# Kernel tuning notes

Hardware: AMD Instinct MI355X
Metric: run time of the kernel (lower is better)

The kernel has to match this reference:

```python
import jax, jax.numpy as jnp
import numpy as np

B = 131072
RES_DIM = 100
N_CHAMBERS = 6
CF_ITERS = 5
CF_K = 0.02

COUPLING = np.array([
    [0.0, -0.3, 0.6, 0.4, -0.2, 0.3],
    [-0.3, 0.0, -0.5, -0.7, 0.6, 0.4],
    [0.6, -0.5, 0.0, 0.3, -0.3, 0.2],
    [0.4, -0.7, 0.3, 0.0, -0.4, 0.5],
    [-0.2, 0.6, -0.3, -0.4, 0.0, 0.3],
    [0.3, 0.4, 0.2, 0.5, 0.3, 0.0],
], dtype=np.float32)
DECAY = np.array([0.9, 0.93, 0.85, 0.97, 0.88, 0.94], dtype=np.float32)


def setup_inputs() -> dict:
    key = jax.random.key(0)
    ks = jax.random.split(key, 9)
    def lin(k, fan_in, fan_out):
        kw, kb = jax.random.split(k)
        bound = 1.0 / np.sqrt(fan_in)
        W = jax.random.uniform(kw, (N_CHAMBERS, fan_in, fan_out), jnp.float32, -bound, bound)
        b = jax.random.uniform(kb, (N_CHAMBERS, fan_out), jnp.float32, -bound, bound)
        return W, b
    W1, b1 = lin(ks[0], RES_DIM, 128)
    W2, b2 = lin(ks[1], 128, 64)
    W3, b3 = lin(ks[2], 64, 32)
    W4, b4 = lin(ks[3], 32, 1)
    W4 = W4[:, :, 0]  # (6, 32)
    b4 = b4[:, 0]     # (6,)
    res = jax.random.normal(ks[4], (B, RES_DIM), jnp.float32)
    return {
        "res": res,
        "W1": W1, "b1": b1, "W2": W2, "b2": b2,
        "W3": W3, "b3": b3, "W4": W4, "b4": b4,
        "coupling": jnp.asarray(COUPLING),
        "decay": jnp.asarray(DECAY),
    }


def reference(res, W1, b1, W2, b2, W3, b3, W4, b4, coupling, decay):
    # 6 per-chamber MLP towers, batched over the chamber axis c.
    h = jax.nn.silu(jnp.einsum('bd,cdh->cbh', res, W1) + b1[:, None, :])   # (6,B,128)
    h = jax.nn.silu(jnp.einsum('cbh,cho->cbo', h, W2) + b2[:, None, :])    # (6,B,64)
    h = jax.nn.silu(jnp.einsum('cbh,cho->cbo', h, W3) + b3[:, None, :])    # (6,B,32)
    raw = (jnp.einsum('cbh,ch->cb', h, W4) + b4[:, None]).T                # (B,6)
    # 5-step coupled sigmoid recurrence on the tiny (B,6) state.
    act = jax.nn.sigmoid(raw)
    for _ in range(CF_ITERS):
        delta = ((act * decay) @ coupling) * CF_K
        act = jax.nn.sigmoid(raw + delta)
    return act, raw
```

## Files before the change

### kernel.cpp

```cpp
#include <hip/hip_runtime.h>
#include <hip/hip_bf16.h>
#include <stdint.h>

#define B_TOTAL 131072

typedef __attribute__((ext_vector_type(8))) short short8;
typedef __attribute__((ext_vector_type(16))) float float16v;

#define CH_U16 24576
#define oF2 14336
#define oF3 22528
#define BF16_TOT (6 * CH_U16)
#define F32_BASE (BF16_TOT / 2)
#define sB1 0
#define sB2 768
#define sB3 1152
#define sW4 1344
#define sB4 1536
#define sCP 1542
#define sDC 1578
#define NSMALL 1584
#define CONV_TOT (BF16_TOT + NSMALL)

#define GLB_AS __attribute__((address_space(1)))
#define LDS_AS __attribute__((address_space(3)))

__device__ __forceinline__ float bf16_as_f32(uint16_t u) {
    union { uint32_t i; float f; } v; v.i = ((uint32_t)u) << 16; return v.f;
}
__device__ __forceinline__ uint16_t f2bf(float f) {
    uint32_t u = __float_as_uint(f);
    return (uint16_t)((u + 0x7FFFu + ((u >> 16) & 1u)) >> 16);
}
__device__ __forceinline__ float sigmoidf_fast(float x) {
    return __builtin_amdgcn_rcpf(1.0f + __expf(-x));
}
__device__ __forceinline__ float siluf(float x) { return x * sigmoidf_fast(x); }

__device__ __forceinline__ float readsrc(const void* p, int off, bool bf) {
    return bf ? bf16_as_f32(((const uint16_t*)p)[off]) : ((const float*)p)[off];
}

__device__ __forceinline__ uint32_t cvtpk_bf16(float lo, float hi) {
    uint32_t r;
    asm("v_cvt_pk_bf16_f32 %0, %1, %2" : "=v"(r) : "v"(lo), "v"(hi));
    return r;
}
__device__ __forceinline__ void plane32swap(uint32_t& a, uint32_t& b) {
    asm("v_permlane32_swap_b32 %0, %1" : "+v"(a), "+v"(b));
}

__global__ void convert_kernel(const void* W1, const void* b1, const void* W2, const void* b2,
                               const void* W3, const void* b3, const void* W4, const void* b4,
                               const void* cp, const void* dc, uint16_t* __restrict__ wsb) {
    const bool bf = (((const uint32_t*)cp)[0] != 0u);
    int idx = blockIdx.x * 256 + threadIdx.x;
    if (idx >= CONV_TOT) return;
    if (idx < BF16_TOT) {
        int c = idx / CH_U16;
        int r = idx - c * CH_U16;
        float v;
        if (r < oF2) {
            int f = r >> 9, rem = r & 511, l = rem >> 3, e = rem & 7;
            int ct = f / 7, kb = f - ct * 7;
            int n = ct * 32 + (l & 31), k = kb * 16 + (l >> 5) * 8 + e;
            v = (k < 100) ? readsrc(W1, c * 12800 + k * 128 + n, bf) : 0.0f;
        } else if (r < oF3) {
            int j = r - oF2;
            int f = j >> 9, rem = j & 511, l = rem >> 3, e = rem & 7;
            int ct2 = f >> 3, kb = f & 7;
            int n = ct2 * 32 + (l & 31), k = kb * 16 + (l >> 5) * 8 + e;
            v = readsrc(W2, c * 8192 + k * 64 + n, bf);
        } else {
            int j = r - oF3;
            int kb = j >> 9, rem = j & 511, l = rem >> 3, e = rem & 7;
            int n = (l & 31), k = kb * 16 + (l >> 5) * 8 + e;
            v = readsrc(W3, c * 2048 + k * 32 + n, bf);
        }
        wsb[idx] = f2bf(v);
    } else {
        int fi = idx - BF16_TOT;
        float v;
        if      (fi < sB2)  v = readsrc(b1, fi, bf);
        else if (fi < sB3)  v = readsrc(b2, fi - sB2, bf);
        else if (fi < sW4)  v = readsrc(b3, fi - sB3, bf);
        else if (fi < sB4)  v = readsrc(W4, fi - sW4, bf);
        else if (fi < sCP)  v = readsrc(b4, fi - sB4, bf);
        else if (fi < sDC)  v = readsrc(cp, fi - sCP, bf);
        else                v = readsrc(dc, fi - sDC, bf);
        ((float*)wsb)[F32_BASE + fi] = v;
    }
}

union Frag { uint4 u4; uint2 u2[2]; uint32_t u[4]; short8 s8; uint16_t h[8]; };

#define Z16 {0.f,0.f,0.f,0.f,0.f,0.f,0.f,0.f,0.f,0.f,0.f,0.f,0.f,0.f,0.f,0.f}

__global__ __launch_bounds__(512, 4)
void chambers_mfma(const void* __restrict__ resv, const uint16_t* __restrict__ wsb,
                   const uint32_t* __restrict__ cpw, float* __restrict__ outF) {
    const float* wsf = (const float*)wsb;
    const bool bfin = (cpw[0] != 0u);
    const int tid = threadIdx.x;
    const int w = tid >> 6, l = tid & 63;
    const int l5 = l & 31, q2 = l >> 5;
    const int row = blockIdx.x * 256 + w * 32 + l5;

    __shared__ __align__(16) uint16_t sW[CH_U16];
    __shared__ __align__(16) float sB[NSMALL];

    for (int i = tid; i < NSMALL; i += 512) sB[i] = wsf[F32_BASE + i];

    Frag R[7];
    if (bfin) {
        const uint16_t* bp = (const uint16_t*)resv + (size_t)row * 100;
#pragma unroll
        for (int kb = 0; kb < 6; ++kb) {
            const int k0 = kb * 16 + q2 * 8;
            R[kb].u2[0] = *(const uint2*)(bp + k0);
            R[kb].u2[1] = *(const uint2*)(bp + k0 + 4);
        }
        R[6].u4 = make_uint4(0, 0, 0, 0);
        if (q2 == 0) R[6].u2[0] = *(const uint2*)(bp + 96);
    } else {
        const float* fp = (const float*)resv + (size_t)row * 100;
#pragma unroll
        for (int kb = 0; kb < 6; ++kb) {
            const int k0 = kb * 16 + q2 * 8;
            float4 x0 = *(const float4*)(fp + k0);
            float4 x1 = *(const float4*)(fp + k0 + 4);
            R[kb].u[0] = cvtpk_bf16(x0.x, x0.y);
            R[kb].u[1] = cvtpk_bf16(x0.z, x0.w);
            R[kb].u[2] = cvtpk_bf16(x1.x, x1.y);
            R[kb].u[3] = cvtpk_bf16(x1.z, x1.w);
        }
        R[6].u4 = make_uint4(0, 0, 0, 0);
        if (q2 == 0) {
            float4 x0 = *(const float4*)(fp + 96);
            R[6].u[0] = cvtpk_bf16(x0.x, x0.y);
            R[6].u[1] = cvtpk_bf16(x0.z, x0.w);
        }
    }

    float raw0 = 0.f, raw1 = 0.f, raw2 = 0.f, raw3 = 0.f, raw4 = 0.f, raw5 = 0.f;
    uint32_t pk1[16][2];
    uint32_t pk2[8][2];

#pragma unroll 1
    for (int c = 0; c < 6; ++c) {
        if (c) __syncthreads();
        {
            const uint16_t* gsrc = wsb + c * CH_U16;
#pragma unroll
            for (int r = 0; r < 6; ++r) {
                const int chunk = r * 8 + w;
                __builtin_amdgcn_global_load_lds(
                    (const GLB_AS uint32_t*)(gsrc + chunk * 512 + l * 8),
                    (LDS_AS uint32_t*)(sW + chunk * 512),
                    16, 0, 0);
            }
        }
        __syncthreads();

#pragma unroll
        for (int ct = 0; ct < 4; ++ct) {
            float16v acc = Z16;
#pragma unroll
            for (int kb = 0; kb < 7; ++kb) {
                Frag Af; Af.u4 = *(const uint4*)(sW + ((ct * 7 + kb) * 64 + l) * 8);
                acc = __builtin_amdgcn_mfma_f32_32x32x16_bf16(Af.s8, R[kb].s8, acc, 0, 0, 0);
            }
#pragma unroll
            for (int ar = 0; ar < 4; ++ar) {
                const float4 bv = *(const float4*)(sB + sB1 + c * 128 + ct * 32 + ar * 8 + q2 * 4);
                pk1[ct * 4 + ar][0] = cvtpk_bf16(siluf(acc[4 * ar + 0] + bv.x),
                                                 siluf(acc[4 * ar + 1] + bv.y));
                pk1[ct * 4 + ar][1] = cvtpk_bf16(siluf(acc[4 * ar + 2] + bv.z),
                                                 siluf(acc[4 * ar + 3] + bv.w));
            }
        }
#pragma unroll
        for (int ct2 = 0; ct2 < 2; ++ct2) {
            float16v acc = Z16;
#pragma unroll
            for (int kb = 0; kb < 8; ++kb) {
                uint32_t x0 = pk1[2 * kb][0], y0 = pk1[2 * kb + 1][0];
                uint32_t x1 = pk1[2 * kb][1], y1 = pk1[2 * kb + 1][1];
                plane32swap(x0, y0);
                plane32swap(x1, y1);
                Frag Hf; Hf.u[0] = x0; Hf.u[1] = x1; Hf.u[2] = y0; Hf.u[3] = y1;
                Frag Af; Af.u4 = *(const uint4*)(sW + oF2 + ((ct2 * 8 + kb) * 64 + l) * 8);
                acc = __builtin_amdgcn_mfma_f32_32x32x16_bf16(Af.s8, Hf.s8, acc, 0, 0, 0);
            }
#pragma unroll
            for (int ar = 0; ar < 4; ++ar) {
                const float4 bv = *(const float4*)(sB + sB2 + c * 64 + ct2 * 32 + ar * 8 + q2 * 4);
                pk2[ct2 * 4 + ar][0] = cvtpk_bf16(siluf(acc[4 * ar + 0] + bv.x),
                                                  siluf(acc[4 * ar + 1] + bv.y));
                pk2[ct2 * 4 + ar][1] = cvtpk_bf16(siluf(acc[4 * ar + 2] + bv.z),
                                                  siluf(acc[4 * ar + 3] + bv.w));
            }
        }
        {
            float16v acc = Z16;
#pragma unroll
            for (int kb = 0; kb < 4; ++kb) {
                uint32_t x0 = pk2[2 * kb][0], y0 = pk2[2 * kb + 1][0];
                uint32_t x1 = pk2[2 * kb][1], y1 = pk2[2 * kb + 1][1];
                plane32swap(x0, y0);
                plane32swap(x1, y1);
                Frag Hf; Hf.u[0] = x0; Hf.u[1] = x1; Hf.u[2] = y0; Hf.u[3] = y1;
                Frag Af; Af.u4 = *(const uint4*)(sW + oF3 + (kb * 64 + l) * 8);
                acc = __builtin_amdgcn_mfma_f32_32x32x16_bf16(Af.s8, Hf.s8, acc, 0, 0, 0);
            }
            float part = 0.f;
#pragma unroll
            for (int ar = 0; ar < 4; ++ar) {
                const float4 bv = *(const float4*)(sB + sB3 + c * 32 + ar * 8 + q2 * 4);
                const float4 wv = *(const float4*)(sB + sW4 + c * 32 + ar * 8 + q2 * 4);
                part = fmaf(siluf(acc[4 * ar + 0] + bv.x), wv.x, part);
                part = fmaf(siluf(acc[4 * ar + 1] + bv.y), wv.y, part);
                part = fmaf(siluf(acc[4 * ar + 2] + bv.z), wv.z, part);
                part = fmaf(siluf(acc[4 * ar + 3] + bv.w), wv.w, part);
            }
            part += __shfl_xor(part, 32);
            const float rv = part + sB[sB4 + c];
            raw0 = (c == 0) ? rv : raw0;
            raw1 = (c == 1) ? rv : raw1;
            raw2 = (c == 2) ? rv : raw2;
            raw3 = (c == 3) ? rv : raw3;
            raw4 = (c == 4) ? rv : raw4;
            raw5 = (c == 5) ? rv : raw5;
        }
    }

    const float rv6[6] = {raw0, raw1, raw2, raw3, raw4, raw5};
    float av[6];
#pragma unroll
    for (int c = 0; c < 6; ++c) av[c] = sigmoidf_fast(rv6[c]);
    const float K = 0.02f;
#pragma unroll 1
    for (int it = 0; it < 5; ++it) {
        float tt[6];
#pragma unroll
        for (int i = 0; i < 6; ++i) tt[i] = av[i] * sB[sDC + i] * K;
#pragma unroll
        for (int j = 0; j < 6; ++j) {
            float dl = 0.0f;
#pragma unroll
            for (int i = 0; i < 6; ++i) dl = fmaf(tt[i], sB[sCP + i * 6 + j], dl);
            av[j] = sigmoidf_fast(rv6[j] + dl);
        }
    }
    if (q2 == 0) {
        float2* oa = (float2*)(outF + (size_t)row * 6);
        oa[0] = make_float2(av[0], av[1]);
        oa[1] = make_float2(av[2], av[3]);
        oa[2] = make_float2(av[4], av[5]);
        float2* orw = (float2*)(outF + (size_t)B_TOTAL * 6 + (size_t)row * 6);
        orw[0] = make_float2(rv6[0], rv6[1]);
        orw[1] = make_float2(rv6[2], rv6[3]);
        orw[2] = make_float2(rv6[4], rv6[5]);
    }
}

extern "C" void kernel_launch(void* const* d_in, const int* in_sizes, int n_in,
                              void* d_out, int out_size, void* d_ws, size_t ws_size,
                              hipStream_t stream) {
    uint16_t* wsb = (uint16_t*)d_ws;
    convert_kernel<<<(CONV_TOT + 255) / 256, 256, 0, stream>>>(
        d_in[1], d_in[2], d_in[3], d_in[4], d_in[5], d_in[6], d_in[7], d_in[8],
        d_in[9], d_in[10], wsb);
    chambers_mfma<<<B_TOTAL / 256, 512, 0, stream>>>(
        d_in[0], wsb, (const uint32_t*)d_in[9], (float*)d_out);
}
```

Before: 163.5 us.

## Load layer-2 weights directly from global into registers and seed accumulators with biases

Layer-2 weight fragments now go straight from global memory (L2-cached) into registers instead of being staged through LDS. LDS staging is cut to layer-1 and layer-3 weights, which shrinks shared memory from 48KB to 32KB per block. MFMA accumulators are initialised with the bias values, so the bias adds after each GEMM go away. The aim is to lower LDS traffic and footprint, which could allow more resident blocks. The cost is more VGPR pressure from 8 live uint4 fragments and global-load latency inside the chamber loop.

```diff
diff --git a/kernel.cpp b/kernel.cpp
--- a/kernel.cpp
+++ b/kernel.cpp
@@ -21,6 +21,8 @@
 #define sDC 1578
 #define NSMALL 1584
 #define CONV_TOT (BF16_TOT + NSMALL)
+
+#define sWF3 14336
 
 #define GLB_AS __attribute__((address_space(1)))
 #define LDS_AS __attribute__((address_space(3)))
@@ -94,8 +96,6 @@
 
 union Frag { uint4 u4; uint2 u2[2]; uint32_t u[4]; short8 s8; uint16_t h[8]; };
 
-#define Z16 {0.f,0.f,0.f,0.f,0.f,0.f,0.f,0.f,0.f,0.f,0.f,0.f,0.f,0.f,0.f,0.f}
-
 __global__ __launch_bounds__(512, 4)
 void chambers_mfma(const void* __restrict__ resv, const uint16_t* __restrict__ wsb,
                    const uint32_t* __restrict__ cpw, float* __restrict__ outF) {
@@ -106,7 +106,7 @@
     const int l5 = l & 31, q2 = l >> 5;
     const int row = blockIdx.x * 256 + w * 32 + l5;
 
-    __shared__ __align__(16) uint16_t sW[CH_U16];
+    __shared__ __align__(16) uint16_t sW[16384];
     __shared__ __align__(16) float sB[NSMALL];
 
     for (int i = tid; i < NSMALL; i += 512) sB[i] = wsf[F32_BASE + i];
@@ -152,19 +152,32 @@
         {
             const uint16_t* gsrc = wsb + c * CH_U16;
 #pragma unroll
-            for (int r = 0; r < 6; ++r) {
-                const int chunk = r * 8 + w;
+            for (int r = 0; r < 4; ++r) {
+                const int i = r * 8 + w;
+                const int gi = (i < 28) ? i : (i + 16);
                 __builtin_amdgcn_global_load_lds(
-                    (const GLB_AS uint32_t*)(gsrc + chunk * 512 + l * 8),
-                    (LDS_AS uint32_t*)(sW + chunk * 512),
+                    (const GLB_AS uint32_t*)(gsrc + gi * 512 + l * 8),
+                    (LDS_AS uint32_t*)(sW + i * 512),
                     16, 0, 0);
             }
         }
         __syncthreads();
 
+        const uint16_t* gF2 = wsb + c * CH_U16 + oF2;
+        Frag F2a[8];
+#pragma unroll
+        for (int kb = 0; kb < 8; ++kb)
+            F2a[kb].u4 = *(const uint4*)(gF2 + (kb * 64 + l) * 8);
+
 #pragma unroll
         for (int ct = 0; ct < 4; ++ct) {
-            float16v acc = Z16;
+            float16v acc;
+#pragma unroll
+            for (int ar = 0; ar < 4; ++ar) {
+                const float4 bv = *(const float4*)(sB + sB1 + c * 128 + ct * 32 + ar * 8 + q2 * 4);
+                acc[4 * ar + 0] = bv.x; acc[4 * ar + 1] = bv.y;
+                acc[4 * ar + 2] = bv.z; acc[4 * ar + 3] = bv.w;
+            }
 #pragma unroll
             for (int kb = 0; kb < 7; ++kb) {
                 Frag Af; Af.u4 = *(const uint4*)(sW + ((ct * 7 + kb) * 64 + l) * 8);
@@ -172,37 +185,56 @@
             }
 #pragma unroll
             for (int ar = 0; ar < 4; ++ar) {
-                const float4 bv = *(const float4*)(sB + sB1 + c * 128 + ct * 32 + ar * 8 + q2 * 4);
-                pk1[ct * 4 + ar][0] = cvtpk_bf16(siluf(acc[4 * ar + 0] + bv.x),
-                                                 siluf(acc[4 * ar + 1] + bv.y));
-                pk1[ct * 4 + ar][1] = cvtpk_bf16(siluf(acc[4 * ar + 2] + bv.z),
-                                                 siluf(acc[4 * ar + 3] + bv.w));
-            }
-        }
-#pragma unroll
-        for (int ct2 = 0; ct2 < 2; ++ct2) {
-            float16v acc = Z16;
-#pragma unroll
-            for (int kb = 0; kb < 8; ++kb) {
-                uint32_t x0 = pk1[2 * kb][0], y0 = pk1[2 * kb + 1][0];
-                uint32_t x1 = pk1[2 * kb][1], y1 = pk1[2 * kb + 1][1];
-                plane32swap(x0, y0);
-                plane32swap(x1, y1);
-                Frag Hf; Hf.u[0] = x0; Hf.u[1] = x1; Hf.u[2] = y0; Hf.u[3] = y1;
-                Frag Af; Af.u4 = *(const uint4*)(sW + oF2 + ((ct2 * 8 + kb) * 64 + l) * 8);
-                acc = __builtin_amdgcn_mfma_f32_32x32x16_bf16(Af.s8, Hf.s8, acc, 0, 0, 0);
-            }
+                pk1[ct * 4 + ar][0] = cvtpk_bf16(siluf(acc[4 * ar + 0]),
+                                                 siluf(acc[4 * ar + 1]));
+                pk1[ct * 4 + ar][1] = cvtpk_bf16(siluf(acc[4 * ar + 2]),
+                                                 siluf(acc[4 * ar + 3]));
+            }
+        }
+
+        Frag F2b[8];
+#pragma unroll
+        for (int kb = 0; kb < 8; ++kb)
+            F2b[kb].u4 = *(const uint4*)(gF2 + ((8 + kb) * 64 + l) * 8);
+
+#define L2_TILE(F2R, CT2)                                                              \
+        {                                                                              \
+            float16v acc;                                                              \
+            _Pragma("unroll")                                                          \
+            for (int ar = 0; ar < 4; ++ar) {                                           \
+                const float4 bv = *(const float4*)(sB + sB2 + c * 64 + (CT2) * 32 + ar * 8 + q2 * 4); \
+                acc[4 * ar + 0] = bv.x; acc[4 * ar + 1] = bv.y;                        \
+                acc[4 * ar + 2] = bv.z; acc[4 * ar + 3] = bv.w;                        \
+            }                                                                          \
+            _Pragma("unroll")                                                          \
+            for (int kb = 0; kb < 8; ++kb) {                                           \
+                uint32_t x0 = pk1[2 * kb][0], y0 = pk1[2 * kb + 1][0];                 \
+                uint32_t x1 = pk1[2 * kb][1], y1 = pk1[2 * kb + 1][1];                 \
+                plane32swap(x0, y0);                                                   \
+                plane32swap(x1, y1);                                                   \
+                Frag Hf; Hf.u[0] = x0; Hf.u[1] = x1; Hf.u[2] = y0; Hf.u[3] = y1;       \
+                acc = __builtin_amdgcn_mfma_f32_32x32x16_bf16(F2R[kb].s8, Hf.s8, acc, 0, 0, 0); \
+            }                                                                          \
+            _Pragma("unroll")                                                          \
+            for (int ar = 0; ar < 4; ++ar) {                                           \
+                pk2[(CT2) * 4 + ar][0] = cvtpk_bf16(siluf(acc[4 * ar + 0]),            \
+                                                    siluf(acc[4 * ar + 1]));           \
+                pk2[(CT2) * 4 + ar][1] = cvtpk_bf16(siluf(acc[4 * ar + 2]),            \
+                                                    siluf(acc[4 * ar + 3]));           \
+            }                                                                          \
+        }
+        L2_TILE(F2a, 0)
+        L2_TILE(F2b, 1)
+#undef L2_TILE
+
+        {
+            float16v acc;
 #pragma unroll
             for (int ar = 0; ar < 4; ++ar) {
-                const float4 bv = *(const float4*)(sB + sB2 + c * 64 + ct2 * 32 + ar * 8 + q2 * 4);
-                pk2[ct2 * 4 + ar][0] = cvtpk_bf16(siluf(acc[4 * ar + 0] + bv.x),
-                                                  siluf(acc[4 * ar + 1] + bv.y));
-                pk2[ct2 * 4 + ar][1] = cvtpk_bf16(siluf(acc[4 * ar + 2] + bv.z),
-                                                  siluf(acc[4 * ar + 3] + bv.w));
-            }
-        }
-        {
-            float16v acc = Z16;
+                const float4 bv = *(const float4*)(sB + sB3 + c * 32 + ar * 8 + q2 * 4);
+                acc[4 * ar + 0] = bv.x; acc[4 * ar + 1] = bv.y;
+                acc[4 * ar + 2] = bv.z; acc[4 * ar + 3] = bv.w;
+            }
 #pragma unroll
             for (int kb = 0; kb < 4; ++kb) {
                 uint32_t x0 = pk2[2 * kb][0], y0 = pk2[2 * kb + 1][0];
@@ -210,18 +242,17 @@
                 plane32swap(x0, y0);
                 plane32swap(x1, y1);
                 Frag Hf; Hf.u[0] = x0; Hf.u[1] = x1; Hf.u[2] = y0; Hf.u[3] = y1;
-                Frag Af; Af.u4 = *(const uint4*)(sW + oF3 + (kb * 64 + l) * 8);
+                Frag Af; Af.u4 = *(const uint4*)(sW + sWF3 + (kb * 64 + l) * 8);
                 acc = __builtin_amdgcn_mfma_f32_32x32x16_bf16(Af.s8, Hf.s8, acc, 0, 0, 0);
             }
             float part = 0.f;
 #pragma unroll
             for (int ar = 0; ar < 4; ++ar) {
-                const float4 bv = *(const float4*)(sB + sB3 + c * 32 + ar * 8 + q2 * 4);
                 const float4 wv = *(const float4*)(sB + sW4 + c * 32 + ar * 8 + q2 * 4);
-                part = fmaf(siluf(acc[4 * ar + 0] + bv.x), wv.x, part);
-                part = fmaf(siluf(acc[4 * ar + 1] + bv.y), wv.y, part);
-                part = fmaf(siluf(acc[4 * ar + 2] + bv.z), wv.z, part);
-                part = fmaf(siluf(acc[4 * ar + 3] + bv.w), wv.w, part);
+                part = fmaf(siluf(acc[4 * ar + 0]), wv.x, part);
+                part = fmaf(siluf(acc[4 * ar + 1]), wv.y, part);
+                part = fmaf(siluf(acc[4 * ar + 2]), wv.z, part);
+                part = fmaf(siluf(acc[4 * ar + 3]), wv.w, part);
             }
             part += __shfl_xor(part, 32);
             const float rv = part + sB[sB4 + c];
```

Result: no change. 161.4 us (-1.3%).

## Double-buffer chamber weights in LDS and read W2 directly from global

Applied to the files above, without the earlier changes.

Stages only the W1 and W3 fragments of each chamber into one of two LDS buffers. The next chamber's load is issued while the current chamber computes, which hides the weight-fetch latency and removes one barrier per chamber. W2 fragments are now read straight from global memory through the cache instead of LDS. Biases are preloaded into the MFMA accumulators, so no separate add is needed after the matmul. The trade-offs are a larger LDS footprint and extra global/L1 traffic for W2 on the critical MFMA path.

```diff
diff --git a/kernel.cpp b/kernel.cpp
--- a/kernel.cpp
+++ b/kernel.cpp
@@ -22,6 +22,9 @@
 #define NSMALL 1584
 #define CONV_TOT (BF16_TOT + NSMALL)
 
+#define sWF3 14336
+#define BUF_U16 16384
+
 #define GLB_AS __attribute__((address_space(1)))
 #define LDS_AS __attribute__((address_space(3)))
 
@@ -45,6 +48,9 @@
     uint32_t r;
     asm("v_cvt_pk_bf16_f32 %0, %1, %2" : "=v"(r) : "v"(lo), "v"(hi));
     return r;
+}
+__device__ __forceinline__ uint32_t silu2bf(float a, float b) {
+    return cvtpk_bf16(siluf(a), siluf(b));
 }
 __device__ __forceinline__ void plane32swap(uint32_t& a, uint32_t& b) {
     asm("v_permlane32_swap_b32 %0, %1" : "+v"(a), "+v"(b));
@@ -94,8 +100,6 @@
 
 union Frag { uint4 u4; uint2 u2[2]; uint32_t u[4]; short8 s8; uint16_t h[8]; };
 
-#define Z16 {0.f,0.f,0.f,0.f,0.f,0.f,0.f,0.f,0.f,0.f,0.f,0.f,0.f,0.f,0.f,0.f}
-
 __global__ __launch_bounds__(512, 4)
 void chambers_mfma(const void* __restrict__ resv, const uint16_t* __restrict__ wsb,
                    const uint32_t* __restrict__ cpw, float* __restrict__ outF) {
@@ -106,8 +110,24 @@
     const int l5 = l & 31, q2 = l >> 5;
     const int row = blockIdx.x * 256 + w * 32 + l5;
 
-    __shared__ __align__(16) uint16_t sW[CH_U16];
+    __shared__ __align__(16) uint16_t sW[2 * BUF_U16];
     __shared__ __align__(16) float sB[NSMALL];
+
+#define STAGE(CC)                                                              \
+    {                                                                          \
+        const uint16_t* gsrc = wsb + (CC) * CH_U16;                            \
+        uint16_t* ldst = sW + ((CC) & 1) * BUF_U16;                            \
+        _Pragma("unroll")                                                      \
+        for (int r = 0; r < 4; ++r) {                                          \
+            const int i = r * 8 + w;                                           \
+            const int gi = (i < 28) ? i : (i + 16);                            \
+            __builtin_amdgcn_global_load_lds(                                  \
+                (const GLB_AS uint32_t*)(gsrc + gi * 512 + l * 8),             \
+                (LDS_AS uint32_t*)(ldst + i * 512), 16, 0, 0);                 \
+        }                                                                      \
+    }
+
+    STAGE(0)
 
     for (int i = tid; i < NSMALL; i += 512) sB[i] = wsf[F32_BASE + i];
 
@@ -142,46 +162,48 @@
         }
     }
 
+    __syncthreads();
+
     float raw0 = 0.f, raw1 = 0.f, raw2 = 0.f, raw3 = 0.f, raw4 = 0.f, raw5 = 0.f;
     uint32_t pk1[16][2];
     uint32_t pk2[8][2];
 
 #pragma unroll 1
     for (int c = 0; c < 6; ++c) {
-        if (c) __syncthreads();
-        {
-            const uint16_t* gsrc = wsb + c * CH_U16;
-#pragma unroll
-            for (int r = 0; r < 6; ++r) {
-                const int chunk = r * 8 + w;
-                __builtin_amdgcn_global_load_lds(
-                    (const GLB_AS uint32_t*)(gsrc + chunk * 512 + l * 8),
-                    (LDS_AS uint32_t*)(sW + chunk * 512),
-                    16, 0, 0);
-            }
-        }
-        __syncthreads();
+        const uint16_t* const bufc = sW + (c & 1) * BUF_U16;
+        if (c < 5) STAGE(c + 1)
 
 #pragma unroll
         for (int ct = 0; ct < 4; ++ct) {
-            float16v acc = Z16;
+            float16v acc;
+#pragma unroll
+            for (int ar = 0; ar < 4; ++ar) {
+                const float4 bv = *(const float4*)(sB + sB1 + c * 128 + ct * 32 + ar * 8 + q2 * 4);
+                acc[4 * ar + 0] = bv.x; acc[4 * ar + 1] = bv.y;
+                acc[4 * ar + 2] = bv.z; acc[4 * ar + 3] = bv.w;
+            }
 #pragma unroll
             for (int kb = 0; kb < 7; ++kb) {
-                Frag Af; Af.u4 = *(const uint4*)(sW + ((ct * 7 + kb) * 64 + l) * 8);
+                Frag Af; Af.u4 = *(const uint4*)(bufc + ((ct * 7 + kb) * 64 + l) * 8);
                 acc = __builtin_amdgcn_mfma_f32_32x32x16_bf16(Af.s8, R[kb].s8, acc, 0, 0, 0);
             }
 #pragma unroll
             for (int ar = 0; ar < 4; ++ar) {
-                const float4 bv = *(const float4*)(sB + sB1 + c * 128 + ct * 32 + ar * 8 + q2 * 4);
-                pk1[ct * 4 + ar][0] = cvtpk_bf16(siluf(acc[4 * ar + 0] + bv.x),
-                                                 siluf(acc[4 * ar + 1] + bv.y));
-                pk1[ct * 4 + ar][1] = cvtpk_bf16(siluf(acc[4 * ar + 2] + bv.z),
-                                                 siluf(acc[4 * ar + 3] + bv.w));
-            }
-        }
+                pk1[ct * 4 + ar][0] = silu2bf(acc[4 * ar + 0], acc[4 * ar + 1]);
+                pk1[ct * 4 + ar][1] = silu2bf(acc[4 * ar + 2], acc[4 * ar + 3]);
+            }
+        }
+
+        const uint16_t* gF2 = wsb + c * CH_U16 + oF2;
 #pragma unroll
         for (int ct2 = 0; ct2 < 2; ++ct2) {
-            float16v acc = Z16;
+            float16v acc;
+#pragma unroll
+            for (int ar = 0; ar < 4; ++ar) {
+                const float4 bv = *(const float4*)(sB + sB2 + c * 64 + ct2 * 32 + ar * 8 + q2 * 4);
+                acc[4 * ar + 0] = bv.x; acc[4 * ar + 1] = bv.y;
+                acc[4 * ar + 2] = bv.z; acc[4 * ar + 3] = bv.w;
+            }
 #pragma unroll
             for (int kb = 0; kb < 8; ++kb) {
                 uint32_t x0 = pk1[2 * kb][0], y0 = pk1[2 * kb + 1][0];
@@ -189,20 +211,24 @@
                 plane32swap(x0, y0);
                 plane32swap(x1, y1);
                 Frag Hf; Hf.u[0] = x0; Hf.u[1] = x1; Hf.u[2] = y0; Hf.u[3] = y1;
-                Frag Af; Af.u4 = *(const uint4*)(sW + oF2 + ((ct2 * 8 + kb) * 64 + l) * 8);
+                Frag Af; Af.u4 = *(const uint4*)(gF2 + ((ct2 * 8 + kb) * 64 + l) * 8);
                 acc = __builtin_amdgcn_mfma_f32_32x32x16_bf16(Af.s8, Hf.s8, acc, 0, 0, 0);
             }
 #pragma unroll
             for (int ar = 0; ar < 4; ++ar) {
-                const float4 bv = *(const float4*)(sB + sB2 + c * 64 + ct2 * 32 + ar * 8 + q2 * 4);
-                pk2[ct2 * 4 + ar][0] = cvtpk_bf16(siluf(acc[4 * ar + 0] + bv.x),
-                                                  siluf(acc[4 * ar + 1] + bv.y));
-                pk2[ct2 * 4 + ar][1] = cvtpk_bf16(siluf(acc[4 * ar + 2] + bv.z),
-                                                  siluf(acc[4 * ar + 3] + bv.w));
-            }
-        }
+                pk2[ct2 * 4 + ar][0] = silu2bf(acc[4 * ar + 0], acc[4 * ar + 1]);
+                pk2[ct2 * 4 + ar][1] = silu2bf(acc[4 * ar + 2], acc[4 * ar + 3]);
+            }
+        }
+
         {
-            float16v acc = Z16;
+            float16v acc;
+#pragma unroll
+            for (int ar = 0; ar < 4; ++ar) {
+                const float4 bv = *(const float4*)(sB + sB3 + c * 32 + ar * 8 + q2 * 4);
+                acc[4 * ar + 0] = bv.x; acc[4 * ar + 1] = bv.y;
+                acc[4 * ar + 2] = bv.z; acc[4 * ar + 3] = bv.w;
+            }
 #pragma unroll
             for (int kb = 0; kb < 4; ++kb) {
                 uint32_t x0 = pk2[2 * kb][0], y0 = pk2[2 * kb + 1][0];
@@ -210,18 +236,17 @@
                 plane32swap(x0, y0);
                 plane32swap(x1, y1);
                 Frag Hf; Hf.u[0] = x0; Hf.u[1] = x1; Hf.u[2] = y0; Hf.u[3] = y1;
-                Frag Af; Af.u4 = *(const uint4*)(sW + oF3 + (kb * 64 + l) * 8);
+                Frag Af; Af.u4 = *(const uint4*)(bufc + sWF3 + (kb * 64 + l) * 8);
                 acc = __builtin_amdgcn_mfma_f32_32x32x16_bf16(Af.s8, Hf.s8, acc, 0, 0, 0);
             }
             float part = 0.f;
 #pragma unroll
             for (int ar = 0; ar < 4; ++ar) {
-                const float4 bv = *(const float4*)(sB + sB3 + c * 32 + ar * 8 + q2 * 4);
                 const float4 wv = *(const float4*)(sB + sW4 + c * 32 + ar * 8 + q2 * 4);
-                part = fmaf(siluf(acc[4 * ar + 0] + bv.x), wv.x, part);
-                part = fmaf(siluf(acc[4 * ar + 1] + bv.y), wv.y, part);
-                part = fmaf(siluf(acc[4 * ar + 2] + bv.z), wv.z, part);
-                part = fmaf(siluf(acc[4 * ar + 3] + bv.w), wv.w, part);
+                part = fmaf(siluf(acc[4 * ar + 0]), wv.x, part);
+                part = fmaf(siluf(acc[4 * ar + 1]), wv.y, part);
+                part = fmaf(siluf(acc[4 * ar + 2]), wv.z, part);
+                part = fmaf(siluf(acc[4 * ar + 3]), wv.w, part);
             }
             part += __shfl_xor(part, 32);
             const float rv = part + sB[sB4 + c];
@@ -232,6 +257,8 @@
             raw4 = (c == 4) ? rv : raw4;
             raw5 = (c == 5) ? rv : raw5;
         }
+
+        if (c < 5) __syncthreads();
     }
 
     const float rv6[6] = {raw0, raw1, raw2, raw3, raw4, raw5};
@@ -262,6 +289,7 @@
         orw[1] = make_float2(rv6[2], rv6[3]);
         orw[2] = make_float2(rv6[4], rv6[5]);
     }
+#undef STAGE
 }
 
 extern "C" void kernel_launch(void* const* d_in, const int* in_sizes, int n_in,
```

Result: no change. 165.9 us (+1.4%).

## Switch tower MLP to 16x16x32 MFMA tiles with smaller blocks

Applied to the files above, without the earlier changes.

Replaces the 32x32x16 MFMA tiling with 16x16x32 tiles and reorders the weight fragments to match. The layer-1 to layer-2 hand-off no longer needs permlane swaps, and biases are folded into the accumulator init. Each block now covers 128 rows, stages only layer-1 weights in LDS, and reads layer-2/3 weights straight from global memory. Occupancy is raised to 8 waves-per-EU, at the cost of per-block weight reuse, global loads in the inner loop, and an extra shuffle reduction.

```diff
diff --git a/kernel.cpp b/kernel.cpp
--- a/kernel.cpp
+++ b/kernel.cpp
@@ -5,11 +5,11 @@
 #define B_TOTAL 131072
 
 typedef __attribute__((ext_vector_type(8))) short short8;
-typedef __attribute__((ext_vector_type(16))) float float16v;
-
-#define CH_U16 24576
-#define oF2 14336
-#define oF3 22528
+typedef __attribute__((ext_vector_type(4))) float float4v;
+
+#define CH_U16 26624
+#define oF2 16384
+#define oF3 24576
 #define BF16_TOT (6 * CH_U16)
 #define F32_BASE (BF16_TOT / 2)
 #define sB1 0
@@ -46,8 +46,8 @@
     asm("v_cvt_pk_bf16_f32 %0, %1, %2" : "=v"(r) : "v"(lo), "v"(hi));
     return r;
 }
-__device__ __forceinline__ void plane32swap(uint32_t& a, uint32_t& b) {
-    asm("v_permlane32_swap_b32 %0, %1" : "+v"(a), "+v"(b));
+__device__ __forceinline__ uint32_t silu2bf(float a, float b) {
+    return cvtpk_bf16(siluf(a), siluf(b));
 }
 
 __global__ void convert_kernel(const void* W1, const void* b1, const void* W2, const void* b2,
@@ -62,19 +62,23 @@
         float v;
         if (r < oF2) {
             int f = r >> 9, rem = r & 511, l = rem >> 3, e = rem & 7;
-            int ct = f / 7, kb = f - ct * 7;
-            int n = ct * 32 + (l & 31), k = kb * 16 + (l >> 5) * 8 + e;
+            int nt = f >> 2, kb = f & 3;
+            int n = nt * 16 + (l & 15);
+            int k = kb * 32 + (l >> 4) * 8 + e;
             v = (k < 100) ? readsrc(W1, c * 12800 + k * 128 + n, bf) : 0.0f;
         } else if (r < oF3) {
             int j = r - oF2;
             int f = j >> 9, rem = j & 511, l = rem >> 3, e = rem & 7;
-            int ct2 = f >> 3, kb = f & 7;
-            int n = ct2 * 32 + (l & 31), k = kb * 16 + (l >> 5) * 8 + e;
+            int nt2 = f >> 2, kb = f & 3;
+            int n = nt2 * 16 + (l & 15);
+            int k = kb * 32 + 16 * (e >> 2) + 4 * (l >> 4) + (e & 3);
             v = readsrc(W2, c * 8192 + k * 64 + n, bf);
         } else {
             int j = r - oF3;
-            int kb = j >> 9, rem = j & 511, l = rem >> 3, e = rem & 7;
-            int n = (l & 31), k = kb * 16 + (l >> 5) * 8 + e;
+            int f = j >> 9, rem = j & 511, l = rem >> 3, e = rem & 7;
+            int nt3 = f >> 1, kb = f & 1;
+            int n = nt3 * 16 + (l & 15);
+            int k = kb * 32 + 16 * (e >> 2) + 4 * (l >> 4) + (e & 3);
             v = readsrc(W3, c * 2048 + k * 32 + n, bf);
         }
         wsb[idx] = f2bf(v);
@@ -94,39 +98,50 @@
 
 union Frag { uint4 u4; uint2 u2[2]; uint32_t u[4]; short8 s8; uint16_t h[8]; };
 
-#define Z16 {0.f,0.f,0.f,0.f,0.f,0.f,0.f,0.f,0.f,0.f,0.f,0.f,0.f,0.f,0.f,0.f}
-
-__global__ __launch_bounds__(512, 4)
+__global__ __launch_bounds__(512, 8)
 void chambers_mfma(const void* __restrict__ resv, const uint16_t* __restrict__ wsb,
                    const uint32_t* __restrict__ cpw, float* __restrict__ outF) {
     const float* wsf = (const float*)wsb;
     const bool bfin = (cpw[0] != 0u);
     const int tid = threadIdx.x;
     const int w = tid >> 6, l = tid & 63;
-    const int l5 = l & 31, q2 = l >> 5;
-    const int row = blockIdx.x * 256 + w * 32 + l5;
-
-    __shared__ __align__(16) uint16_t sW[CH_U16];
+    const int r4 = l & 15, q4 = l >> 4;
+    const int row = blockIdx.x * 128 + w * 16 + r4;
+
+    __shared__ __align__(16) uint16_t sW[16384];
     __shared__ __align__(16) float sB[NSMALL];
 
+#define STAGE(CC)                                                              \
+    {                                                                          \
+        const uint16_t* gsrc = wsb + (CC) * CH_U16;                            \
+        _Pragma("unroll")                                                      \
+        for (int rr = 0; rr < 4; ++rr) {                                       \
+            const int i = rr * 8 + w;                   \
+            __builtin_amdgcn_global_load_lds(                                  \
+                (const GLB_AS uint32_t*)(gsrc + i * 512 + l * 8),              \
+                (LDS_AS uint32_t*)(sW + i * 512), 16, 0, 0);                   \
+        }                                                                      \
+    }
+
+    STAGE(0)
     for (int i = tid; i < NSMALL; i += 512) sB[i] = wsf[F32_BASE + i];
 
-    Frag R[7];
+    Frag R[3], R3;
+    R3.u4 = make_uint4(0, 0, 0, 0);
     if (bfin) {
         const uint16_t* bp = (const uint16_t*)resv + (size_t)row * 100;
 #pragma unroll
-        for (int kb = 0; kb < 6; ++kb) {
-            const int k0 = kb * 16 + q2 * 8;
+        for (int kb = 0; kb < 3; ++kb) {
+            const int k0 = kb * 32 + q4 * 8;
             R[kb].u2[0] = *(const uint2*)(bp + k0);
             R[kb].u2[1] = *(const uint2*)(bp + k0 + 4);
         }
-        R[6].u4 = make_uint4(0, 0, 0, 0);
-        if (q2 == 0) R[6].u2[0] = *(const uint2*)(bp + 96);
+        if (q4 == 0) R3.u2[0] = *(const uint2*)(bp + 96);
     } else {
         const float* fp = (const float*)resv + (size_t)row * 100;
 #pragma unroll
-        for (int kb = 0; kb < 6; ++kb) {
-            const int k0 = kb * 16 + q2 * 8;
+        for (int kb = 0; kb < 3; ++kb) {
+            const int k0 = kb * 32 + q4 * 8;
             float4 x0 = *(const float4*)(fp + k0);
             float4 x1 = *(const float4*)(fp + k0 + 4);
             R[kb].u[0] = cvtpk_bf16(x0.x, x0.y);
@@ -134,103 +149,99 @@
             R[kb].u[2] = cvtpk_bf16(x1.x, x1.y);
             R[kb].u[3] = cvtpk_bf16(x1.z, x1.w);
         }
-        R[6].u4 = make_uint4(0, 0, 0, 0);
-        if (q2 == 0) {
+        if (q4 == 0) {
             float4 x0 = *(const float4*)(fp + 96);
-            R[6].u[0] = cvtpk_bf16(x0.x, x0.y);
-            R[6].u[1] = cvtpk_bf16(x0.z, x0.w);
-        }
-    }
+            R3.u[0] = cvtpk_bf16(x0.x, x0.y);
+            R3.u[1] = cvtpk_bf16(x0.z, x0.w);
+        }
+    }
+
+    __syncthreads();
 
     float raw0 = 0.f, raw1 = 0.f, raw2 = 0.f, raw3 = 0.f, raw4 = 0.f, raw5 = 0.f;
-    uint32_t pk1[16][2];
-    uint32_t pk2[8][2];
+    uint32_t pk1[8][2];
+    uint32_t pk2[4][2];
 
 #pragma unroll 1
     for (int c = 0; c < 6; ++c) {
-        if (c) __syncthreads();
-        {
-            const uint16_t* gsrc = wsb + c * CH_U16;
-#pragma unroll
-            for (int r = 0; r < 6; ++r) {
-                const int chunk = r * 8 + w;
-                __builtin_amdgcn_global_load_lds(
-                    (const GLB_AS uint32_t*)(gsrc + chunk * 512 + l * 8),
-                    (LDS_AS uint32_t*)(sW + chunk * 512),
-                    16, 0, 0);
-            }
-        }
-        __syncthreads();
-
-#pragma unroll
-        for (int ct = 0; ct < 4; ++ct) {
-            float16v acc = Z16;
-#pragma unroll
-            for (int kb = 0; kb < 7; ++kb) {
-                Frag Af; Af.u4 = *(const uint4*)(sW + ((ct * 7 + kb) * 64 + l) * 8);
-                acc = __builtin_amdgcn_mfma_f32_32x32x16_bf16(Af.s8, R[kb].s8, acc, 0, 0, 0);
-            }
-#pragma unroll
-            for (int ar = 0; ar < 4; ++ar) {
-                const float4 bv = *(const float4*)(sB + sB1 + c * 128 + ct * 32 + ar * 8 + q2 * 4);
-                pk1[ct * 4 + ar][0] = cvtpk_bf16(siluf(acc[4 * ar + 0] + bv.x),
-                                                 siluf(acc[4 * ar + 1] + bv.y));
-                pk1[ct * 4 + ar][1] = cvtpk_bf16(siluf(acc[4 * ar + 2] + bv.z),
-                                                 siluf(acc[4 * ar + 3] + bv.w));
-            }
-        }
-#pragma unroll
-        for (int ct2 = 0; ct2 < 2; ++ct2) {
-            float16v acc = Z16;
-#pragma unroll
-            for (int kb = 0; kb < 8; ++kb) {
-                uint32_t x0 = pk1[2 * kb][0], y0 = pk1[2 * kb + 1][0];
-                uint32_t x1 = pk1[2 * kb][1], y1 = pk1[2 * kb + 1][1];
-                plane32swap(x0, y0);
-                plane32swap(x1, y1);
-                Frag Hf; Hf.u[0] = x0; Hf.u[1] = x1; Hf.u[2] = y0; Hf.u[3] = y1;
-                Frag Af; Af.u4 = *(const uint4*)(sW + oF2 + ((ct2 * 8 + kb) * 64 + l) * 8);
-                acc = __builtin_amdgcn_mfma_f32_32x32x16_bf16(Af.s8, Hf.s8, acc, 0, 0, 0);
-            }
-#pragma unroll
-            for (int ar = 0; ar < 4; ++ar) {
-                const float4 bv = *(const float4*)(sB + sB2 + c * 64 + ct2 * 32 + ar * 8 + q2 * 4);
-                pk2[ct2 * 4 + ar][0] = cvtpk_bf16(siluf(acc[4 * ar + 0] + bv.x),
-                                                  siluf(acc[4 * ar + 1] + bv.y));
-                pk2[ct2 * 4 + ar][1] = cvtpk_bf16(siluf(acc[4 * ar + 2] + bv.z),
-                                                  siluf(acc[4 * ar + 3] + bv.w));
-            }
-        }
-        {
-            float16v acc = Z16;
+#pragma unroll
+        for (int nt = 0; nt < 8; ++nt) {
+            float4v acc;
+            {
+                const float4 bv = *(const float4*)(sB + sB1 + c * 128 + nt * 16 + q4 * 4);
+                acc[0] = bv.x; acc[1] = bv.y; acc[2] = bv.z; acc[3] = bv.w;
+            }
+            const uint16_t* fp1 = sW + (nt * 4) * 512 + l * 8;
+            Frag A0, A1, A2, A3;
+            A0.u4 = *(const uint4*)(fp1);
+            A1.u4 = *(const uint4*)(fp1 + 512);
+            A2.u4 = *(const uint4*)(fp1 + 1024);
+            A3.u4 = *(const uint4*)(fp1 + 1536);
+            acc = __builtin_amdgcn_mfma_f32_16x16x32_bf16(A0.s8, R[0].s8, acc, 0, 0, 0);
+            acc = __builtin_amdgcn_mfma_f32_16x16x32_bf16(A1.s8, R[1].s8, acc, 0, 0, 0);
+            acc = __builtin_amdgcn_mfma_f32_16x16x32_bf16(A2.s8, R[2].s8, acc, 0, 0, 0);
+            acc = __builtin_amdgcn_mfma_f32_16x16x32_bf16(A3.s8, R3.s8,   acc, 0, 0, 0);
+            pk1[nt][0] = silu2bf(acc[0], acc[1]);
+            pk1[nt][1] = silu2bf(acc[2], acc[3]);
+        }
+
+        const uint16_t* gF2 = wsb + c * CH_U16 + oF2;
+#pragma unroll
+        for (int nt2 = 0; nt2 < 4; ++nt2) {
+            float4v acc;
+            {
+                const float4 bv = *(const float4*)(sB + sB2 + c * 64 + nt2 * 16 + q4 * 4);
+                acc[0] = bv.x; acc[1] = bv.y; acc[2] = bv.z; acc[3] = bv.w;
+            }
 #pragma unroll
             for (int kb = 0; kb < 4; ++kb) {
-                uint32_t x0 = pk2[2 * kb][0], y0 = pk2[2 * kb + 1][0];
-                uint32_t x1 = pk2[2 * kb][1], y1 = pk2[2 * kb + 1][1];
-                plane32swap(x0, y0);
-                plane32swap(x1, y1);
-                Frag Hf; Hf.u[0] = x0; Hf.u[1] = x1; Hf.u[2] = y0; Hf.u[3] = y1;
-                Frag Af; Af.u4 = *(const uint4*)(sW + oF3 + (kb * 64 + l) * 8);
-                acc = __builtin_amdgcn_mfma_f32_32x32x16_bf16(Af.s8, Hf.s8, acc, 0, 0, 0);
-            }
-            float part = 0.f;
-#pragma unroll
-            for (int ar = 0; ar < 4; ++ar) {
-                const float4 bv = *(const float4*)(sB + sB3 + c * 32 + ar * 8 + q2 * 4);
-                const float4 wv = *(const float4*)(sB + sW4 + c * 32 + ar * 8 + q2 * 4);
-                part = fmaf(siluf(acc[4 * ar + 0] + bv.x), wv.x, part);
-                part = fmaf(siluf(acc[4 * ar + 1] + bv.y), wv.y, part);
-                part = fmaf(siluf(acc[4 * ar + 2] + bv.z), wv.z, part);
-                part = fmaf(siluf(acc[4 * ar + 3] + bv.w), wv.w, part);
-            }
-            part += __shfl_xor(part, 32);
-            const float rv = part + sB[sB4 + c];
-            raw0 = (c == 0) ? rv : raw0;
-            raw1 = (c == 1) ? rv : raw1;
-            raw2 = (c == 2) ? rv : raw2;
-            raw3 = (c == 3) ? rv : raw3;
-            raw4 = (c == 4) ? rv : raw4;
-            raw5 = (c == 5) ? rv : raw5;
+                Frag Hf;
+                Hf.u[0] = pk1[2 * kb][0];     Hf.u[1] = pk1[2 * kb][1];
+                Hf.u[2] = pk1[2 * kb + 1][0]; Hf.u[3] = pk1[2 * kb + 1][1];
+                Frag Af; Af.u4 = *(const uint4*)(gF2 + ((nt2 * 4 + kb) * 64 + l) * 8);
+                acc = __builtin_amdgcn_mfma_f32_16x16x32_bf16(Af.s8, Hf.s8, acc, 0, 0, 0);
+            }
+            pk2[nt2][0] = silu2bf(acc[0], acc[1]);
+            pk2[nt2][1] = silu2bf(acc[2], acc[3]);
+        }
+
+        const uint16_t* gF3 = wsb + c * CH_U16 + oF3;
+        float part = 0.f;
+#pragma unroll
+        for (int nt3 = 0; nt3 < 2; ++nt3) {
+            float4v acc;
+            {
+                const float4 bv = *(const float4*)(sB + sB3 + c * 32 + nt3 * 16 + q4 * 4);
+                acc[0] = bv.x; acc[1] = bv.y; acc[2] = bv.z; acc[3] = bv.w;
+            }
+#pragma unroll
+            for (int kb = 0; kb < 2; ++kb) {
+                Frag Hf;
+                Hf.u[0] = pk2[2 * kb][0];     Hf.u[1] = pk2[2 * kb][1];
+                Hf.u[2] = pk2[2 * kb + 1][0]; Hf.u[3] = pk2[2 * kb + 1][1];
+                Frag Af; Af.u4 = *(const uint4*)(gF3 + ((nt3 * 2 + kb) * 64 + l) * 8);
+                acc = __builtin_amdgcn_mfma_f32_16x16x32_bf16(Af.s8, Hf.s8, acc, 0, 0, 0);
+            }
+            const float4 wv = *(const float4*)(sB + sW4 + c * 32 + nt3 * 16 + q4 * 4);
+            part = fmaf(siluf(acc[0]), wv.x, part);
+            part = fmaf(siluf(acc[1]), wv.y, part);
+            part = fmaf(siluf(acc[2]), wv.z, part);
+            part = fmaf(siluf(acc[3]), wv.w, part);
+        }
+        part += __shfl_xor(part, 16);
+        part += __shfl_xor(part, 32);
+        const float rv = part + sB[sB4 + c];
+        raw0 = (c == 0) ? rv : raw0;
+        raw1 = (c == 1) ? rv : raw1;
+        raw2 = (c == 2) ? rv : raw2;
+        raw3 = (c == 3) ? rv : raw3;
+        raw4 = (c == 4) ? rv : raw4;
+        raw5 = (c == 5) ? rv : raw5;
+
+        if (c < 5) {
+            __syncthreads();
+            STAGE(c + 1)
+            __syncthreads();
         }
     }
 
@@ -252,7 +263,7 @@
             av[j] = sigmoidf_fast(rv6[j] + dl);
         }
     }
-    if (q2 == 0) {
+    if (q4 == 0) {
         float2* oa = (float2*)(outF + (size_t)row * 6);
         oa[0] = make_float2(av[0], av[1]);
         oa[1] = make_float2(av[2], av[3]);
@@ -262,6 +273,7 @@
         orw[1] = make_float2(rv6[2], rv6[3]);
         orw[2] = make_float2(rv6[4], rv6[5]);
     }
+#undef STAGE
 }
 
 extern "C" void kernel_launch(void* const* d_in, const int* in_sizes, int n_in,
@@ -271,6 +283,6 @@
     convert_kernel<<<(CONV_TOT + 255) / 256, 256, 0, stream>>>(
         d_in[1], d_in[2], d_in[3], d_in[4], d_in[5], d_in[6], d_in[7], d_in[8],
         d_in[9], d_in[10], wsb);
-    chambers_mfma<<<B_TOTAL / 256, 512, 0, stream>>>(
+    chambers_mfma<<<B_TOTAL / 128, 512, 0, stream>>>(
         d_in[0], wsb, (const uint32_t*)d_in[9], (float*)d_out);
 }
```

Measured after the change: 206.3 us. +26.1%, slower.
